# Kernel optimization log

Hardware: AMD Instinct MI355X
Metric: run time of the kernel (lower is better)

Reference implementation:

```python
import jax, jax.numpy as jnp
import numpy as np

B, D, H, C = 512, 1024, 512, 4


def setup_inputs() -> dict:
    key = jax.random.key(0)
    k_x, k_v, k_w = jax.random.split(key, 3)
    # x holds categorical values in [0, C) used as float multipliers
    x = jax.random.randint(k_x, (B, D), 0, C).astype(jnp.float32)
    # xavier_normal_ per torch fan computation: V fan_in=D*C, fan_out=H*C; W fan_in=D, fan_out=H
    V = jax.random.normal(k_v, (H, D, C), jnp.float32) * np.float32(np.sqrt(2.0 / (D * C + H * C)))
    b = jnp.zeros((D, C), jnp.float32)
    W = jax.random.normal(k_w, (H, D), jnp.float32) * np.float32(np.sqrt(2.0 / (D + H)))
    c = jnp.zeros((1, H), jnp.float32)
    return {"x": x, "V": V, "b": b, "W": W, "c": c}


def _nade_forward(x, V, b, W, c):
    Bsz = x.shape[0]
    a0 = jnp.broadcast_to(c, (Bsz, c.shape[1]))  # [B, H]
    # per-step slices stacked along leading D axis for lax.scan
    xs = (jnp.transpose(V, (1, 0, 2)),  # [D, H, C]
          b,                            # [D, C]
          W.T,                          # [D, H]
          x.T)                          # [D, B]

    def step(a, inp):
        V_d, b_d, w_d, x_d = inp
        h = jax.nn.sigmoid(a)                 # [B, H]
        logits = h @ V_d + b_d                # [B, C]
        p = jax.nn.log_softmax(logits, axis=1)
        a_new = a + x_d[:, None] * w_d[None, :]  # rank-1 update of running preactivation
        return a_new, (logits, p)

    _, (logits, p) = jax.lax.scan(step, a0, xs)   # each [D, B, C]
    y_hat = jnp.transpose(logits, (1, 0, 2)).reshape(Bsz, -1)  # [B, D*C], d-major blocks of size C
    p_hat = jnp.transpose(p, (1, 0, 2)).reshape(Bsz, -1)
    return y_hat, p_hat


def reference(x, V, b, W, c):
    return _nade_forward(x, V, b, W, c)
```

## Files before the change

### kernel.cpp

```cpp
#include <hip/hip_runtime.h>


#define Bv 512
#define Dv 1024
#define Hv 512
#define Cv 4
#define Kv 32
#define DCv 32

#define L2E 1.4426950408889634f
#define LN2 0.6931471805599453f

typedef __attribute__((ext_vector_type(8))) short short8;
typedef __attribute__((ext_vector_type(4))) float f32x4;

__device__ __forceinline__ float fexp2(float x) { return __builtin_amdgcn_exp2f(x); }
__device__ __forceinline__ float flog2(float x) { return __builtin_amdgcn_logf(x); }
__device__ __forceinline__ float frcp(float x)  { return __builtin_amdgcn_rcpf(x); }

__device__ __forceinline__ unsigned bf16pk(float lo, float hi) {
    return __builtin_amdgcn_perm(__float_as_uint(hi), __float_as_uint(lo), 0x07060302u);
}
__device__ __forceinline__ unsigned short bf16rne(float f) {
    unsigned u = __float_as_uint(f);
    return (unsigned short)((u + 0x7FFFu + ((u >> 16) & 1u)) >> 16);
}

__global__ void k_prep(const float* __restrict__ W, const float* __restrict__ x,
                       float* __restrict__ WtL, float* __restrict__ xt) {
    int gid = blockIdx.x * blockDim.x + threadIdx.x;
    int h = gid & (Hv - 1);
    int d = gid >> 9;
    WtL[(size_t)d * Hv + h] = W[(size_t)h * Dv + d] * L2E;
    xt[(size_t)d * Bv + h]  = x[(size_t)h * Dv + d];
}

__global__ __launch_bounds__(256) void k_prepv(const float* __restrict__ V,
                                               unsigned short* __restrict__ VtA4) {
    __shared__ unsigned short tile[16 * 16 * 16 * 8];
    int d0   = blockIdx.x * 16;
    int hloc = threadIdx.x >> 4;
    int dd   = threadIdx.x & 15;
    for (int pass = 0; pass < 32; ++pass) {
        int h = pass * 16 + hloc;
        float4 v = *(const float4*)(V + ((size_t)h * Dv + d0 + dd) * Cv);
        int hb = h >> 5, q = (h >> 3) & 3, j = h & 7;
        int base = ((dd * 16 + hb) * 16 + q * 4) * 8 + j;
        tile[base + 0 * 8] = bf16rne(v.x);
        tile[base + 1 * 8] = bf16rne(v.y);
        tile[base + 2 * 8] = bf16rne(v.z);
        tile[base + 3 * 8] = bf16rne(v.w);
    }
    __syncthreads();
    uint4* dst = (uint4*)(VtA4 + (size_t)d0 * 16 * 16 * 8);
    const uint4* src = (const uint4*)tile;
    for (int t = threadIdx.x; t < 4096; t += 256) dst[t] = src[t];
}

__global__ __launch_bounds__(512) void k_partial(const float* __restrict__ x,
                          const float* __restrict__ WtL, float* __restrict__ A0) {
    int k  = blockIdx.x >> 6;
    int bg = blockIdx.x & 63;
    int h  = threadIdx.x;
    int d0 = k * DCv;

    __shared__ float xs[DCv * 8];
    if (threadIdx.x < DCv * 8) {
        int g = threadIdx.x >> 5;
        int j = threadIdx.x & 31;
        xs[j * 8 + g] = x[(size_t)(bg * 8 + g) * Dv + d0 + j];
    }
    __syncthreads();

    float acc[8];
#pragma unroll
    for (int g = 0; g < 8; ++g) acc[g] = 0.0f;

    const float* wp = WtL + (size_t)d0 * Hv + h;
    for (int j = 0; j < DCv; ++j) {
        float wv = wp[(size_t)j * Hv];
        const float4 x0 = *(const float4*)(xs + j * 8);
        const float4 x1 = *(const float4*)(xs + j * 8 + 4);
        acc[0] = fmaf(x0.x, wv, acc[0]);
        acc[1] = fmaf(x0.y, wv, acc[1]);
        acc[2] = fmaf(x0.z, wv, acc[2]);
        acc[3] = fmaf(x0.w, wv, acc[3]);
        acc[4] = fmaf(x1.x, wv, acc[4]);
        acc[5] = fmaf(x1.y, wv, acc[5]);
        acc[6] = fmaf(x1.z, wv, acc[6]);
        acc[7] = fmaf(x1.w, wv, acc[7]);
    }
#pragma unroll
    for (int g = 0; g < 8; ++g)
        A0[((size_t)k * Bv + bg * 8 + g) * Hv + h] = acc[g];
}

__global__ void k_prefix(float* __restrict__ A0, const float* __restrict__ cbias) {
    int gid = blockIdx.x * blockDim.x + threadIdx.x;
    int h = gid & (Hv - 1);
    int bi = gid >> 9;
    float run = cbias[h] * L2E;
    float* p = A0 + (size_t)bi * Hv + h;
    for (int k = 0; k < Kv; ++k) {
        float t = p[(size_t)k * Bv * Hv];
        p[(size_t)k * Bv * Hv] = run;
        run += t;
    }
}

__global__ __launch_bounds__(256, 4) void k_main(
        const float* __restrict__ xt, const float* __restrict__ bbias,
        const unsigned short* __restrict__ VtA4, const float* __restrict__ WtL,
        const float* __restrict__ A0, float* __restrict__ out) {
    const int k    = blockIdx.x >> 5;
    const int bg   = blockIdx.x & 31;
    const int wid  = threadIdx.x >> 6;
    const int lane = threadIdx.x & 63;
    const int bl   = lane & 15;
    const int quad = lane >> 4;
    const int b    = bg * 16 + bl;
    const int d0   = k * DCv;

    __shared__ f32x4 red[2][4][64];

    float a[32];
    {
        const float* ap = A0 + ((size_t)k * Bv + b) * Hv + wid * 128 + quad * 8;
#pragma unroll
        for (int kb = 0; kb < 4; ++kb) {
            float4 t0 = *(const float4*)(ap + kb * 32);
            float4 t1 = *(const float4*)(ap + kb * 32 + 4);
            a[kb*8+0]=t0.x; a[kb*8+1]=t0.y; a[kb*8+2]=t0.z; a[kb*8+3]=t0.w;
            a[kb*8+4]=t1.x; a[kb*8+5]=t1.y; a[kb*8+6]=t1.z; a[kb*8+7]=t1.w;
        }
    }

    const bool act = (bl < 4);
    const unsigned short* vp = VtA4 + (((size_t)d0 * 16 + wid * 4) * 16 + quad * 4 + bl) * 8;
    const float* wp = WtL + (size_t)d0 * Hv + wid * 128 + quad * 8;
    const float* xp = xt + (size_t)d0 * Bv + b;
    const float* bp = bbias + d0 * Cv;
    float* yp = out + (size_t)b * Dv * Cv + d0 * Cv;
    float* pp = yp + (size_t)Bv * Dv * Cv;

    const short8 zfrag = {0,0,0,0,0,0,0,0};

    for (int i = 0; i < DCv; ++i) {
        short8 af[4];
#pragma unroll
        for (int kb = 0; kb < 4; ++kb)
            af[kb] = act ? *(const short8*)(vp + kb * 128) : zfrag;
        float xd = xp[0];
        float4 bbv = *(const float4*)bp;

        unsigned pk[16];
#pragma unroll
        for (int m = 0; m < 32; m += 2) {
            float s0 = frcp(1.0f + fexp2(-a[m]));
            float s1 = frcp(1.0f + fexp2(-a[m + 1]));
            pk[m >> 1] = bf16pk(s0, s1);
        }

#pragma unroll
        for (int kb = 0; kb < 4; ++kb)
#pragma unroll
            for (int j = 0; j < 8; ++j)
                a[kb*8+j] = fmaf(xd, wp[kb*32+j], a[kb*8+j]);

        f32x4 acc = {0.f, 0.f, 0.f, 0.f};
#pragma unroll
        for (int kb = 0; kb < 4; ++kb) {
            union { unsigned u[4]; short8 s; } cv;
            cv.u[0] = pk[kb*4+0]; cv.u[1] = pk[kb*4+1];
            cv.u[2] = pk[kb*4+2]; cv.u[3] = pk[kb*4+3];
            acc = __builtin_amdgcn_mfma_f32_16x16x32_bf16(af[kb], cv.s, acc, 0, 0, 0);
        }

        red[i & 1][wid][lane] = acc;
        __syncthreads();
        f32x4 r0 = red[i & 1][0][lane];
        f32x4 r1 = red[i & 1][1][lane];
        f32x4 r2 = red[i & 1][2][lane];
        f32x4 r3 = red[i & 1][3][lane];
        float w0 = r0.x + r1.x + r2.x + r3.x + bbv.x;
        float w1 = r0.y + r1.y + r2.y + r3.y + bbv.y;
        float w2 = r0.z + r1.z + r2.z + r3.z + bbv.z;
        float w3 = r0.w + r1.w + r2.w + r3.w + bbv.w;

        float mx = fmaxf(fmaxf(w0, w1), fmaxf(w2, w3));
        float e0 = fexp2((w0 - mx) * L2E);
        float e1 = fexp2((w1 - mx) * L2E);
        float e2 = fexp2((w2 - mx) * L2E);
        float e3 = fexp2((w3 - mx) * L2E);
        float lse = mx + flog2(e0 + e1 + e2 + e3) * LN2;

        if (quad == 0) {
            if (wid == 0) {
                *(float4*)yp = make_float4(w0, w1, w2, w3);
            } else if (wid == 1) {
                *(float4*)pp = make_float4(w0 - lse, w1 - lse, w2 - lse, w3 - lse);
            }
        }

        vp += 16 * 16 * 8;
        wp += Hv;
        xp += Bv;
        bp += Cv;
        yp += Cv;
        pp += Cv;
    }
}

extern "C" void kernel_launch(void* const* d_in, const int* in_sizes, int n_in,
                              void* d_out, int out_size, void* d_ws, size_t ws_size,
                              hipStream_t stream) {
    const float* x  = (const float*)d_in[0];
    const float* V  = (const float*)d_in[1];
    const float* bb = (const float*)d_in[2];
    const float* W  = (const float*)d_in[3];
    const float* cb = (const float*)d_in[4];
    float* out = (float*)d_out;

    char* ws = (char*)d_ws;
    unsigned short* VtA4 = (unsigned short*)ws;
    float* WtL = (float*)(ws + (size_t)4 * 1024 * 1024);
    float* xt  = (float*)(ws + (size_t)6 * 1024 * 1024);
    float* A0  = (float*)(ws + (size_t)8 * 1024 * 1024);

    k_prep<<<(Hv * Dv) / 256, 256, 0, stream>>>(W, x, WtL, xt);
    k_prepv<<<Dv / 16, 256, 0, stream>>>(V, VtA4);
    k_partial<<<Kv * (Bv / 8), 512, 0, stream>>>(x, WtL, A0);
    k_prefix<<<(Bv * Hv) / 256, 256, 0, stream>>>(A0, cb);
    k_main<<<Kv * 32, 256, 0, stream>>>(xt, bb, VtA4, WtL, A0, out);
}
```

Before: 184.4 us.

## Process two steps per barrier in main kernel; tile transposes in prep kernels

The main kernel now computes two consecutive d-steps per loop iteration, which halves the number of block-wide barriers. It also splits the epilogue so that waves 0/2 store logits and waves 1/3 compute and store the log-softmax for each of the two steps. The W/x transpose prep is replaced by a shared-memory tiled transpose with coalesced float4 accesses, and the V repack uses four d per block, giving more blocks. The cost is more registers, from the doubled A fragments and packed sigmoids, which may reduce occupancy.

```diff
diff --git a/kernel.cpp b/kernel.cpp
--- a/kernel.cpp
+++ b/kernel.cpp
@@ -26,23 +26,51 @@
     return (unsigned short)((u + 0x7FFFu + ((u >> 16) & 1u)) >> 16);
 }
 
-__global__ void k_prep(const float* __restrict__ W, const float* __restrict__ x,
-                       float* __restrict__ WtL, float* __restrict__ xt) {
-    int gid = blockIdx.x * blockDim.x + threadIdx.x;
-    int h = gid & (Hv - 1);
-    int d = gid >> 9;
-    WtL[(size_t)d * Hv + h] = W[(size_t)h * Dv + d] * L2E;
-    xt[(size_t)d * Bv + h]  = x[(size_t)h * Dv + d];
+__global__ __launch_bounds__(256) void k_prep(const float* __restrict__ W,
+                                              const float* __restrict__ x,
+                                              float* __restrict__ WtL,
+                                              float* __restrict__ xt) {
+    __shared__ float t[64][65];
+    const int mb   = blockIdx.x >> 7;
+    const int tile = blockIdx.x & 127;
+    const int tr   = tile >> 4;
+    const int tc   = tile & 15;
+    const float* src = mb ? x : W;
+    float* dst       = mb ? xt : WtL;
+    const float scale = mb ? 1.0f : L2E;
+    const int lx = threadIdx.x & 15;
+    const int ly = threadIdx.x >> 4;
+
+#pragma unroll
+    for (int r = 0; r < 64; r += 16) {
+        int row = r + ly;
+        float4 v = *(const float4*)(src + (size_t)(tr * 64 + row) * Dv + tc * 64 + lx * 4);
+        t[row][lx * 4 + 0] = v.x;
+        t[row][lx * 4 + 1] = v.y;
+        t[row][lx * 4 + 2] = v.z;
+        t[row][lx * 4 + 3] = v.w;
+    }
+    __syncthreads();
+#pragma unroll
+    for (int r = 0; r < 64; r += 16) {
+        int row = r + ly;
+        float4 o = make_float4(t[lx * 4 + 0][row] * scale,
+                               t[lx * 4 + 1][row] * scale,
+                               t[lx * 4 + 2][row] * scale,
+                               t[lx * 4 + 3][row] * scale);
+        *(float4*)(dst + (size_t)(tc * 64 + row) * 512 + tr * 64 + lx * 4) = o;
+    }
 }
 
 __global__ __launch_bounds__(256) void k_prepv(const float* __restrict__ V,
                                                unsigned short* __restrict__ VtA4) {
-    __shared__ unsigned short tile[16 * 16 * 16 * 8];
-    int d0   = blockIdx.x * 16;
-    int hloc = threadIdx.x >> 4;
-    int dd   = threadIdx.x & 15;
-    for (int pass = 0; pass < 32; ++pass) {
-        int h = pass * 16 + hloc;
+    __shared__ unsigned short tile[4 * 16 * 16 * 8];
+    const int d0 = blockIdx.x * 4;
+    const int dd = threadIdx.x & 3;
+    const int hb0 = threadIdx.x >> 2;
+#pragma unroll
+    for (int p = 0; p < 8; ++p) {
+        int h = p * 64 + hb0;
         float4 v = *(const float4*)(V + ((size_t)h * Dv + d0 + dd) * Cv);
         int hb = h >> 5, q = (h >> 3) & 3, j = h & 7;
         int base = ((dd * 16 + hb) * 16 + q * 4) * 8 + j;
@@ -52,9 +80,9 @@
         tile[base + 3 * 8] = bf16rne(v.w);
     }
     __syncthreads();
-    uint4* dst = (uint4*)(VtA4 + (size_t)d0 * 16 * 16 * 8);
+    uint4* dst = (uint4*)(VtA4 + (size_t)d0 * 2048);
     const uint4* src = (const uint4*)tile;
-    for (int t = threadIdx.x; t < 4096; t += 256) dst[t] = src[t];
+    for (int tt = threadIdx.x; tt < 1024; tt += 256) dst[tt] = src[tt];
 }
 
 __global__ __launch_bounds__(512) void k_partial(const float* __restrict__ x,
@@ -120,8 +148,10 @@
     const int quad = lane >> 4;
     const int b    = bg * 16 + bl;
     const int d0   = k * DCv;
-
-    __shared__ f32x4 red[2][4][64];
+    const int stp  = wid >> 1;
+    const bool isP = wid & 1;
+
+    __shared__ f32x4 red[2][2][4][64];
 
     float a[32];
     {
@@ -139,75 +169,97 @@
     const unsigned short* vp = VtA4 + (((size_t)d0 * 16 + wid * 4) * 16 + quad * 4 + bl) * 8;
     const float* wp = WtL + (size_t)d0 * Hv + wid * 128 + quad * 8;
     const float* xp = xt + (size_t)d0 * Bv + b;
-    const float* bp = bbias + d0 * Cv;
-    float* yp = out + (size_t)b * Dv * Cv + d0 * Cv;
-    float* pp = yp + (size_t)Bv * Dv * Cv;
+    const float* bp = bbias + (d0 + stp) * Cv;
+    float* sp = out + (isP ? (size_t)Bv * Dv * Cv : (size_t)0)
+                    + (size_t)b * Dv * Cv + (d0 + stp) * Cv;
 
     const short8 zfrag = {0,0,0,0,0,0,0,0};
 
-    for (int i = 0; i < DCv; ++i) {
-        short8 af[4];
-#pragma unroll
-        for (int kb = 0; kb < 4; ++kb)
-            af[kb] = act ? *(const short8*)(vp + kb * 128) : zfrag;
-        float xd = xp[0];
+    for (int i1 = 0; i1 < DCv / 2; ++i1) {
+        short8 afA[4], afB[4];
+#pragma unroll
+        for (int kb = 0; kb < 4; ++kb)
+            afA[kb] = act ? *(const short8*)(vp + kb * 128) : zfrag;
+#pragma unroll
+        for (int kb = 0; kb < 4; ++kb)
+            afB[kb] = act ? *(const short8*)(vp + 2048 + kb * 128) : zfrag;
+        float xdA = xp[0];
+        float xdB = xp[Bv];
         float4 bbv = *(const float4*)bp;
 
-        unsigned pk[16];
+        unsigned pkA[16];
 #pragma unroll
         for (int m = 0; m < 32; m += 2) {
             float s0 = frcp(1.0f + fexp2(-a[m]));
             float s1 = frcp(1.0f + fexp2(-a[m + 1]));
-            pk[m >> 1] = bf16pk(s0, s1);
-        }
-
-#pragma unroll
-        for (int kb = 0; kb < 4; ++kb)
-#pragma unroll
-            for (int j = 0; j < 8; ++j)
-                a[kb*8+j] = fmaf(xd, wp[kb*32+j], a[kb*8+j]);
-
-        f32x4 acc = {0.f, 0.f, 0.f, 0.f};
+            pkA[m >> 1] = bf16pk(s0, s1);
+        }
+        f32x4 accA = {0.f, 0.f, 0.f, 0.f};
 #pragma unroll
         for (int kb = 0; kb < 4; ++kb) {
             union { unsigned u[4]; short8 s; } cv;
-            cv.u[0] = pk[kb*4+0]; cv.u[1] = pk[kb*4+1];
-            cv.u[2] = pk[kb*4+2]; cv.u[3] = pk[kb*4+3];
-            acc = __builtin_amdgcn_mfma_f32_16x16x32_bf16(af[kb], cv.s, acc, 0, 0, 0);
-        }
-
-        red[i & 1][wid][lane] = acc;
+            cv.u[0] = pkA[kb*4+0]; cv.u[1] = pkA[kb*4+1];
+            cv.u[2] = pkA[kb*4+2]; cv.u[3] = pkA[kb*4+3];
+            accA = __builtin_amdgcn_mfma_f32_16x16x32_bf16(afA[kb], cv.s, accA, 0, 0, 0);
+        }
+#pragma unroll
+        for (int kb = 0; kb < 4; ++kb)
+#pragma unroll
+            for (int j = 0; j < 8; ++j)
+                a[kb*8+j] = fmaf(xdA, wp[kb*32+j], a[kb*8+j]);
+
+        unsigned pkB[16];
+#pragma unroll
+        for (int m = 0; m < 32; m += 2) {
+            float s0 = frcp(1.0f + fexp2(-a[m]));
+            float s1 = frcp(1.0f + fexp2(-a[m + 1]));
+            pkB[m >> 1] = bf16pk(s0, s1);
+        }
+        f32x4 accB = {0.f, 0.f, 0.f, 0.f};
+#pragma unroll
+        for (int kb = 0; kb < 4; ++kb) {
+            union { unsigned u[4]; short8 s; } cv;
+            cv.u[0] = pkB[kb*4+0]; cv.u[1] = pkB[kb*4+1];
+            cv.u[2] = pkB[kb*4+2]; cv.u[3] = pkB[kb*4+3];
+            accB = __builtin_amdgcn_mfma_f32_16x16x32_bf16(afB[kb], cv.s, accB, 0, 0, 0);
+        }
+#pragma unroll
+        for (int kb = 0; kb < 4; ++kb)
+#pragma unroll
+            for (int j = 0; j < 8; ++j)
+                a[kb*8+j] = fmaf(xdB, wp[Hv + kb*32+j], a[kb*8+j]);
+
+        red[i1 & 1][0][wid][lane] = accA;
+        red[i1 & 1][1][wid][lane] = accB;
         __syncthreads();
-        f32x4 r0 = red[i & 1][0][lane];
-        f32x4 r1 = red[i & 1][1][lane];
-        f32x4 r2 = red[i & 1][2][lane];
-        f32x4 r3 = red[i & 1][3][lane];
+
+        f32x4 r0 = red[i1 & 1][stp][0][lane];
+        f32x4 r1 = red[i1 & 1][stp][1][lane];
+        f32x4 r2 = red[i1 & 1][stp][2][lane];
+        f32x4 r3 = red[i1 & 1][stp][3][lane];
         float w0 = r0.x + r1.x + r2.x + r3.x + bbv.x;
         float w1 = r0.y + r1.y + r2.y + r3.y + bbv.y;
         float w2 = r0.z + r1.z + r2.z + r3.z + bbv.z;
         float w3 = r0.w + r1.w + r2.w + r3.w + bbv.w;
 
-        float mx = fmaxf(fmaxf(w0, w1), fmaxf(w2, w3));
-        float e0 = fexp2((w0 - mx) * L2E);
-        float e1 = fexp2((w1 - mx) * L2E);
-        float e2 = fexp2((w2 - mx) * L2E);
-        float e3 = fexp2((w3 - mx) * L2E);
-        float lse = mx + flog2(e0 + e1 + e2 + e3) * LN2;
-
-        if (quad == 0) {
-            if (wid == 0) {
-                *(float4*)yp = make_float4(w0, w1, w2, w3);
-            } else if (wid == 1) {
-                *(float4*)pp = make_float4(w0 - lse, w1 - lse, w2 - lse, w3 - lse);
-            }
-        }
-
-        vp += 16 * 16 * 8;
-        wp += Hv;
-        xp += Bv;
-        bp += Cv;
-        yp += Cv;
-        pp += Cv;
+        if (!isP) {
+            if (quad == 0) *(float4*)sp = make_float4(w0, w1, w2, w3);
+        } else {
+            float mx = fmaxf(fmaxf(w0, w1), fmaxf(w2, w3));
+            float e0 = fexp2((w0 - mx) * L2E);
+            float e1 = fexp2((w1 - mx) * L2E);
+            float e2 = fexp2((w2 - mx) * L2E);
+            float e3 = fexp2((w3 - mx) * L2E);
+            float lse = mx + flog2(e0 + e1 + e2 + e3) * LN2;
+            if (quad == 0)
+                *(float4*)sp = make_float4(w0 - lse, w1 - lse, w2 - lse, w3 - lse);
+        }
+
+        vp += 2 * 2048;
+        wp += 2 * Hv;
+        xp += 2 * Bv;
+        bp += 2 * Cv;
+        sp += 2 * Cv;
     }
 }
 
@@ -227,8 +279,8 @@
     float* xt  = (float*)(ws + (size_t)6 * 1024 * 1024);
     float* A0  = (float*)(ws + (size_t)8 * 1024 * 1024);
 
-    k_prep<<<(Hv * Dv) / 256, 256, 0, stream>>>(W, x, WtL, xt);
-    k_prepv<<<Dv / 16, 256, 0, stream>>>(V, VtA4);
+    k_prep<<<256, 256, 0, stream>>>(W, x, WtL, xt);
+    k_prepv<<<Dv / 4, 256, 0, stream>>>(V, VtA4);
     k_partial<<<Kv * (Bv / 8), 512, 0, stream>>>(x, WtL, A0);
     k_prefix<<<(Bv * Hv) / 256, 256, 0, stream>>>(A0, cb);
     k_main<<<Kv * 32, 256, 0, stream>>>(xt, bb, VtA4, WtL, A0, out);
```

Result: faster. 169.5 us (-8.1%).
